# Kernel optimization log

Measured on AMD Instinct MI355X. Metric: run time of the kernel, lower is better.

Reference implementation:

```python
import jax, jax.numpy as jnp
import numpy as np

V = 5023          # FLAME vertex count
NJ = 5            # joints: global, neck, jaw, eyeL, eyeR
N_SHAPE = 100
N_EXP = 50
PARENTS = np.array([-1, 0, 1, 1, 1], dtype=np.int64)  # static kintree
N_BATCH = 2048


def setup_inputs() -> dict:
    key = jax.random.key(0)
    ks = jax.random.split(key, 12)
    N = N_BATCH
    shape = jax.random.normal(ks[0], (N, N_SHAPE), jnp.float32)
    exp = jax.random.normal(ks[1], (N, N_EXP), jnp.float32)
    neck_pose = 0.1 * jax.random.normal(ks[2], (N, 3), jnp.float32)
    jaw_pose = 0.1 * jax.random.normal(ks[3], (N, 3), jnp.float32)
    eye_pose = 0.1 * jax.random.normal(ks[4], (N, 6), jnp.float32)
    v_template = jax.random.normal(ks[5], (V, 3), jnp.float32)
    shapedirs = 0.01 * jax.random.normal(ks[6], (V, 3, N_SHAPE + N_EXP), jnp.float32)
    posedirs = 0.01 * jax.random.normal(ks[7], (36, V * 3), jnp.float32)
    J_regressor = jax.random.uniform(ks[8], (NJ, V), jnp.float32)
    J_regressor = J_regressor / J_regressor.sum(axis=1, keepdims=True)
    lbs_weights = jax.random.uniform(ks[9], (V, NJ), jnp.float32)
    lbs_weights = lbs_weights / lbs_weights.sum(axis=1, keepdims=True)
    parents = jnp.asarray(PARENTS)
    return dict(shape=shape, exp=exp, neck_pose=neck_pose, jaw_pose=jaw_pose,
                eye_pose=eye_pose, v_template=v_template, shapedirs=shapedirs,
                posedirs=posedirs, J_regressor=J_regressor, lbs_weights=lbs_weights,
                parents=parents)


def rodrigues(rot_vecs):
    """Axis-angle [...,3] -> rotation matrices [...,3,3] (matches SMPL/FLAME impl)."""
    angle = jnp.linalg.norm(rot_vecs + 1e-8, axis=-1, keepdims=True)
    rd = rot_vecs / angle
    cos = jnp.cos(angle)[..., None]
    sin = jnp.sin(angle)[..., None]
    rx, ry, rz = rd[..., 0], rd[..., 1], rd[..., 2]
    z = jnp.zeros_like(rx)
    K = jnp.stack([z, -rz, ry, rz, z, -rx, -ry, rx, z], axis=-1).reshape(rd.shape + (3,))
    I = jnp.eye(3, dtype=rot_vecs.dtype)
    return I + sin * K + (1.0 - cos) * (K @ K)


def flame_forward(shape, exp, neck_pose, jaw_pose, eye_pose, v_template,
                  shapedirs, posedirs, J_regressor, lbs_weights):
    N = shape.shape[0]
    dt = shape.dtype
    betas = jnp.concatenate([shape, exp], axis=1)                      # [N,150]
    # full pose: zeroed global rot + neck + jaw + eyes -> [N,NJ,3]
    full_pose = jnp.concatenate([jnp.zeros_like(jaw_pose), neck_pose,
                                 jaw_pose, eye_pose], axis=1).reshape(N, NJ, 3)
    # shape blendshapes
    v_shaped = v_template[None] + jnp.einsum('bl,vkl->bvk', betas, shapedirs)  # [N,V,3]
    J = jnp.einsum('jv,bvk->bjk', J_regressor, v_shaped)               # [N,NJ,3]
    # pose blendshapes
    R = rodrigues(full_pose)                                           # [N,NJ,3,3]
    pose_feature = (R[:, 1:] - jnp.eye(3, dtype=dt)).reshape(N, (NJ - 1) * 9)
    v_posed = v_shaped + (pose_feature @ posedirs).reshape(N, V, 3)
    # kinematic chain (static 5-joint tree)
    rel_J = J.at[:, 1:].add(-J[:, PARENTS[1:]])
    Rt = jnp.concatenate([R, rel_J[..., None]], axis=-1)               # [N,NJ,3,4]
    bottom = jnp.broadcast_to(jnp.array([0., 0., 0., 1.], dtype=dt), (N, NJ, 1, 4))
    T = jnp.concatenate([Rt, bottom], axis=2)                          # [N,NJ,4,4]
    chain = [T[:, 0]]
    for i in range(1, NJ):
        chain.append(chain[int(PARENTS[i])] @ T[:, i])
    G = jnp.stack(chain, axis=1)                                       # [N,NJ,4,4]
    # remove rest-pose joint locations from the transforms
    J_h = jnp.concatenate([J, jnp.zeros((N, NJ, 1), dt)], axis=-1)     # [N,NJ,4]
    t_corr = jnp.einsum('bjrc,bjc->bjr', G, J_h)
    A = G.at[..., 3].add(-t_corr)                                      # [N,NJ,4,4]
    # linear blend skinning
    Tw = jnp.einsum('vj,bjrc->bvrc', lbs_weights, A)                   # [N,V,4,4]
    v_h = jnp.concatenate([v_posed, jnp.ones((N, V, 1), dt)], axis=-1)
    verts = jnp.einsum('bvrc,bvc->bvr', Tw, v_h)[..., :3]              # [N,V,3]
    return verts


def reference(shape, exp, neck_pose, jaw_pose, eye_pose, v_template,
              shapedirs, posedirs, J_regressor, lbs_weights, parents):
    # parents is a static buffer (PARENTS) -- accepted for signature parity.
    return flame_forward(shape, exp, neck_pose, jaw_pose, eye_pose, v_template,
                         shapedirs, posedirs, J_regressor, lbs_weights)
```

## Files before the change

kernel.cpp:

```cpp
#include <hip/hip_runtime.h>
#include <hip/hip_bf16.h>
#include <math.h>

#define NV   5023
#define N3   15069
#define NB   2048
#define NTIL 79
#define NPAD (NTIL*192)

#define WS_JD_B   0
#define WS_ATR_B  9216
#define WS_AB_B   795648
#define WS_BB_B   1582080

#define GP_J 126
#define GP_S 1067
#define GP_P 237

typedef __attribute__((ext_vector_type(8))) short short8;
typedef __attribute__((ext_vector_type(4))) float floatx4;

static __device__ __forceinline__ unsigned short f2bf(float x) {
    union { __hip_bfloat16 h; unsigned short s; } u;
    u.h = __float2bfloat16(x);
    return u.s;
}
static __device__ __forceinline__ unsigned int pk2(float a, float b) {
    return (unsigned int)f2bf(a) | ((unsigned int)f2bf(b) << 16);
}

#define BAR_LGKM() do { \
    asm volatile("s_waitcnt lgkmcnt(0)" ::: "memory"); \
    __builtin_amdgcn_s_barrier(); \
    asm volatile("" ::: "memory"); \
} while (0)

__global__ void k_prep(const float* __restrict__ Jreg,
                       const float* __restrict__ sdirs,
                       const float* __restrict__ vt,
                       const float* __restrict__ pdirs,
                       char* __restrict__ ws) {
    __shared__ float JregL[200];
    __shared__ float PL[36][65];
    const int t = threadIdx.x;

    if (blockIdx.x < GP_J) {
        int slice = blockIdx.x;
        int start = slice * 40;
        int end   = min(start + 40, NV);
        if (t < 200) {
            int j = t / 40, vl = t % 40;
            int v = start + vl;
            JregL[t] = (v < NV) ? Jreg[j * NV + v] : 0.f;
        }
        __syncthreads();
        int s0 = t, s1 = t + 256;
        float a0[5] = {0,0,0,0,0}, a1[5] = {0,0,0,0,0};
        #pragma unroll 2
        for (int v = start; v < end; ++v) {
            int vl = v - start;
            float x0 = (s0 < 450) ? sdirs[(size_t)v * 450 + s0]
                     : (s0 < 453 ? vt[v * 3 + (s0 - 450)] : 0.f);
            float x1 = (s1 < 450) ? sdirs[(size_t)v * 450 + s1]
                     : (s1 < 453 ? vt[v * 3 + (s1 - 450)] : 0.f);
            #pragma unroll
            for (int j = 0; j < 5; ++j) {
                float w = JregL[j * 40 + vl];
                a0[j] += w * x0; a1[j] += w * x1;
            }
        }
        float* Jd = (float*)(ws + WS_JD_B);
        #pragma unroll
        for (int j = 0; j < 5; ++j) {
            if (s0 < 453) atomicAdd(&Jd[j * 453 + s0], a0[j]);
            if (s1 < 453) atomicAdd(&Jd[j * 453 + s1], a1[j]);
        }
    } else if (blockIdx.x < GP_J + GP_S) {
        int idx = (blockIdx.x - GP_J) * 256 + t;
        if (idx < NPAD * 18) {
            int n = idx / 18, g = idx % 18;
            __hip_bfloat16* dst = (__hip_bfloat16*)(ws + WS_BB_B) + (size_t)n * 192 + g * 8;
            if (n < N3) {
                const float* src = sdirs + (size_t)n * 150 + g * 8;
                float2 p0 = *(const float2*)(src);
                float2 p1 = *(const float2*)(src + 2);
                float2 p2 = *(const float2*)(src + 4);
                float2 p3 = *(const float2*)(src + 6);
                unsigned int w[4] = { pk2(p0.x, p0.y), pk2(p1.x, p1.y),
                                      pk2(p2.x, p2.y), pk2(p3.x, p3.y) };
                *(int4*)dst = *(int4*)w;
            } else {
                int4 z = {0, 0, 0, 0};
                *(int4*)dst = z;
            }
        }
    } else {
        int pb = blockIdx.x - (GP_J + GP_S);
        int n0 = pb * 64;
        #pragma unroll
        for (int j = 0; j < 9; ++j) {
            int flat = j * 256 + t;
            int k = flat >> 6, i = flat & 63;
            int n = n0 + i;
            PL[k][i] = (n < N3) ? pdirs[(size_t)k * N3 + n] : 0.f;
        }
        __syncthreads();
        #pragma unroll
        for (int j = 0; j < 2; ++j) {
            int idx2 = j * 256 + t;
            if (idx2 < 384) {
                int r = idx2 / 6, g = idx2 % 6;
                int n = n0 + r;
                int k0 = 144 + g * 8;
                __hip_bfloat16 val[8];
                #pragma unroll
                for (int e = 0; e < 8; ++e) {
                    int k = k0 + e;
                    float v = 0.f;
                    if (k < 150)      v = (n < N3) ? sdirs[(size_t)n * 150 + k] : 0.f;
                    else if (k < 186) v = PL[k - 150][r];
                    val[e] = __float2bfloat16(v);
                }
                *(int4*)((__hip_bfloat16*)(ws + WS_BB_B) + (size_t)n * 192 + k0) = *(int4*)val;
            }
        }
    }
}

static __device__ __forceinline__ void rodr3(float rx, float ry, float rz, float* R) {
    float ax = rx + 1e-8f, ay = ry + 1e-8f, az = rz + 1e-8f;
    float angle = sqrtf(ax*ax + ay*ay + az*az);
    float inv = 1.f / angle;
    float ux = rx * inv, uy = ry * inv, uz = rz * inv;
    float c = cosf(angle), s = sinf(angle);
    float K[9] = {0.f, -uz, uy,  uz, 0.f, -ux,  -uy, ux, 0.f};
    float KK[9];
    #pragma unroll
    for (int r = 0; r < 3; ++r)
        #pragma unroll
        for (int cc = 0; cc < 3; ++cc) {
            float a = 0.f;
            #pragma unroll
            for (int m = 0; m < 3; ++m) a += K[r*3+m] * K[m*3+cc];
            KK[r*3+cc] = a;
        }
    #pragma unroll
    for (int e = 0; e < 9; ++e) R[e] = s * K[e] + (1.f - c) * KK[e];
    R[0] += 1.f; R[4] += 1.f; R[8] += 1.f;
}

#define KBS 0
#define KBE 6464
#define KBJ 9728
#define KBR 11993
#define KBP 16345
#define KBT 18713

__global__ __launch_bounds__(256) void k_batch(
        const float* __restrict__ shp,
        const float* __restrict__ expn,
        const float* __restrict__ neck,
        const float* __restrict__ jaw,
        const float* __restrict__ eye,
        char* __restrict__ ws) {
    __shared__ float L[KBT];
    const int t  = threadIdx.x;
    const int b0 = blockIdx.x * 64;

    {
        const float* Jd = (const float*)(ws + WS_JD_B);
        for (int i = t; i < 6400; i += 256) { int r = i / 100, c = i - r * 100; L[KBS + r*101 + c] = shp[(size_t)b0*100 + i]; }
        for (int i = t; i < 3200; i += 256) { int r = i / 50,  c = i - r * 50;  L[KBE + r*51  + c] = expn[(size_t)b0*50 + i]; }
        for (int i = t; i < 2265; i += 256) L[KBJ + i] = Jd[i];
    }
    __syncthreads();

    const int br = t & 63, seg = t >> 6;
    {
        float Jp[15];
        #pragma unroll
        for (int u = 0; u < 15; ++u) Jp[u] = 0.f;
        int l0 = seg * 38, l1 = (seg == 3) ? 150 : (l0 + 38);
        for (int l = l0; l < l1; ++l) {
            float be = (l < 100) ? L[KBS + br*101 + l] : L[KBE + br*51 + (l - 100)];
            #pragma unroll
            for (int jj = 0; jj < 5; ++jj)
                #pragma unroll
                for (int kk = 0; kk < 3; ++kk)
                    Jp[jj*3 + kk] += L[KBJ + jj*453 + kk*150 + l] * be;
        }
        #pragma unroll
        for (int u = 0; u < 15; ++u) L[KBR + (seg*64 + br)*17 + u] = Jp[u];
    }
    __syncthreads();

    if (t < 64) {
        int b = b0 + t;
        float J[15];
        #pragma unroll
        for (int jk = 0; jk < 15; ++jk) {
            float s = L[KBJ + (jk/3)*453 + 450 + (jk%3)];
            #pragma unroll
            for (int sg = 0; sg < 4; ++sg) s += L[KBR + (sg*64 + t)*17 + jk];
            J[jk] = s;
        }

        float R[4][9];
        rodr3(neck[b*3], neck[b*3+1], neck[b*3+2], R[0]);
        rodr3(jaw[b*3],  jaw[b*3+1],  jaw[b*3+2],  R[1]);
        rodr3(eye[b*6],  eye[b*6+1],  eye[b*6+2],  R[2]);
        rodr3(eye[b*6+3], eye[b*6+4], eye[b*6+5],  R[3]);

        #pragma unroll
        for (int kk2 = 0; kk2 < 4; ++kk2)
            #pragma unroll
            for (int e = 0; e < 9; ++e)
                L[KBP + t*37 + kk2*9 + e] = R[kk2][e] - ((e == 0 || e == 4 || e == 8) ? 1.f : 0.f);

        float* Atr = (float*)(ws + WS_ATR_B) + (size_t)b * 60;
        Atr[0]=1.f; Atr[1]=0.f; Atr[2]=0.f;  Atr[3]=0.f;
        Atr[4]=0.f; Atr[5]=1.f; Atr[6]=0.f;  Atr[7]=0.f;
        Atr[8]=0.f; Atr[9]=0.f; Atr[10]=1.f; Atr[11]=0.f;
        #pragma unroll
        for (int r = 0; r < 3; ++r) {
            float d = R[0][r*3+0]*J[3] + R[0][r*3+1]*J[4] + R[0][r*3+2]*J[5];
            Atr[12 + r*4 + 0] = R[0][r*3+0];
            Atr[12 + r*4 + 1] = R[0][r*3+1];
            Atr[12 + r*4 + 2] = R[0][r*3+2];
            Atr[12 + r*4 + 3] = J[3+r] - d;
        }
        #pragma unroll
        for (int kk = 1; kk < 4; ++kk) {
            int jj = kk + 1;
            float rel[3];
            #pragma unroll
            for (int r = 0; r < 3; ++r) rel[r] = J[jj*3+r] - J[3+r];
            float Gr[9], tv[3];
            #pragma unroll
            for (int r = 0; r < 3; ++r) {
                #pragma unroll
                for (int cc = 0; cc < 3; ++cc) {
                    float a = 0.f;
                    #pragma unroll
                    for (int m = 0; m < 3; ++m) a += R[0][r*3+m] * R[kk][m*3+cc];
                    Gr[r*3+cc] = a;
                }
                tv[r] = R[0][r*3+0]*rel[0] + R[0][r*3+1]*rel[1] + R[0][r*3+2]*rel[2] + J[3+r];
            }
            #pragma unroll
            for (int r = 0; r < 3; ++r) {
                float d = Gr[r*3+0]*J[jj*3+0] + Gr[r*3+1]*J[jj*3+1] + Gr[r*3+2]*J[jj*3+2];
                Atr[jj*12 + r*4 + 0] = Gr[r*3+0];
                Atr[jj*12 + r*4 + 1] = Gr[r*3+1];
                Atr[jj*12 + r*4 + 2] = Gr[r*3+2];
                Atr[jj*12 + r*4 + 3] = tv[r] - d;
            }
        }
    }
    __syncthreads();

    unsigned int* A32g = (unsigned int*)(ws + WS_AB_B);
    for (int i = t; i < 6144; i += 256) {
        int r = i / 96, w = i - r * 96;
        unsigned int val;
        if (w < 50)      val = pk2(L[KBS + r*101 + 2*w],     L[KBS + r*101 + 2*w + 1]);
        else if (w < 75) { int c = 2*(w-50); val = pk2(L[KBE + r*51 + c], L[KBE + r*51 + c + 1]); }
        else if (w < 93) { int c = 2*(w-75); val = pk2(L[KBP + r*37 + c], L[KBP + r*37 + c + 1]); }
        else             val = 0u;
        A32g[(size_t)(b0 + r)*96 + w] = val;
    }
}

#define A_OFF  0
#define B_OFF  4352
#define S_VT   17
#define S_AT   61
#define VT_T_OFF 0
#define ATR_OFF  13056
#define VTQ_OFF  16960
#define LBS_OFF  17728
#define SMEM_BYTES 30464

__global__ __launch_bounds__(256, 5) void k_mega(
        const char* __restrict__ ws,
        const float* __restrict__ vt,
        const float* __restrict__ lbsw,
        float* __restrict__ out) {
    __shared__ __align__(16) unsigned char smem[SMEM_BYTES];
    const unsigned char* AbG = (const unsigned char*)ws + WS_AB_B;
    const unsigned char* BbG = (const unsigned char*)ws + WS_BB_B;
    const float* AtrG = (const float*)(ws + WS_ATR_B);

    const int ntile = blockIdx.y;
    const int b0    = blockIdx.x * 32;
    const int t     = threadIdx.x;
    const int lane  = t & 63;
    const int wn    = t >> 6;
    const int l15 = lane & 15, quad = lane >> 4;

    floatx4 acc[2][3];
    #pragma unroll
    for (int f = 0; f < 2; ++f)
        #pragma unroll
        for (int g = 0; g < 3; ++g) {
            floatx4 z = {0.f, 0.f, 0.f, 0.f};
            acc[f][g] = z;
        }

    for (int chunk = 0; chunk < 3; ++chunk) {
        __syncthreads();
        {
            int row = t >> 3, piece = t & 7;
            *(float4*)(smem + A_OFF + row * 136 + piece * 16) =
                *(const float4*)(AbG + (size_t)(b0 + row) * 384 + chunk * 128 + piece * 16);
        }
        #pragma unroll
        for (int i = 0; i < 6; ++i) {
            int flat = i * 256 + t;
            int row = flat >> 3, piece = flat & 7;
            *(float4*)(smem + B_OFF + row * 136 + piece * 16) =
                *(const float4*)(BbG + (size_t)(ntile * 192 + row) * 384 + chunk * 128 + piece * 16);
        }
        __syncthreads();
        #pragma unroll
        for (int ks = 0; ks < 2; ++ks) {
            short8 af[2];
            #pragma unroll
            for (int f = 0; f < 2; ++f)
                af[f] = *(const short8*)(smem + A_OFF + (f * 16 + l15) * 136 + ks * 64 + quad * 16);
            #pragma unroll
            for (int g = 0; g < 3; ++g) {
                short8 bf = *(const short8*)(smem + B_OFF + (wn * 48 + g * 16 + l15) * 136 + ks * 64 + quad * 16);
                #pragma unroll
                for (int f = 0; f < 2; ++f)
                    acc[f][g] = __builtin_amdgcn_mfma_f32_16x16x32_bf16(af[f], bf, acc[f][g], 0, 0, 0);
            }
        }
    }
    __syncthreads();

    float* vtT  = (float*)(smem + VT_T_OFF);
    float* atrS = (float*)(smem + ATR_OFF);
    float* vtQ  = (float*)(smem + VTQ_OFF);
    float* lbsS = (float*)(smem + LBS_OFF);

    if (t < 192) { int n = ntile * 192 + t; vtQ[t] = (n < N3) ? vt[n] : 0.f; }
    for (int i = t; i < 320; i += 256) {
        int v = ntile * 64 + i / 5;
        lbsS[i] = (v < NV) ? lbsw[(size_t)v * 5 + (i % 5)] : 0.f;
    }
    float arA[4], arB[4];
    #pragma unroll
    for (int u = 0; u < 4; ++u) {
        int i = u * 256 + t;
        arA[u] = (i < 960) ? AtrG[(size_t)b0 * 60 + i] : 0.f;
    }

    #define EPI_PHASE(HH, ARCUR, PRELOAD_NEXT)                                          \
    {                                                                                   \
        BAR_LGKM();                                                                     \
                                   \
        _Pragma("unroll")                                                               \
        for (int g = 0; g < 3; ++g) {                                                   \
            int col = wn * 48 + g * 16 + l15;                                           \
            int rl  = quad * 4;                                                         \
            _Pragma("unroll")                                                           \
            for (int r = 0; r < 4; ++r)                                                 \
                vtT[col * S_VT + rl + r] = acc[HH][g][r];                               \
        }                                                                               \
                                                         \
        _Pragma("unroll")                                                               \
        for (int u = 0; u < 4; ++u) {                                                   \
            int i = u * 256 + t;                                                        \
            if (i < 960) {                                                              \
                int rw = i / 60, cw = i - rw * 60;                                      \
                atrS[rw * S_AT + cw] = ARCUR[u];                                        \
            }                                                                           \
        }                                                                               \
        PRELOAD_NEXT                                                                    \
        BAR_LGKM();                                                                     \
                          \
        {                                                                               \
            int rl = t & 15;                                                            \
            int vgrp = t >> 4;                                                          \
            float ar[60];                                                               \
            _Pragma("unroll")                                                           \
            for (int i = 0; i < 60; ++i) ar[i] = atrS[rl * S_AT + i];                   \
            _Pragma("unroll")                                                           \
            for (int vv = 0; vv < 4; ++vv) {                                            \
                int vloc = vgrp * 4 + vv;                                               \
                int c0 = vloc * 3;                                                      \
                float w0 = lbsS[vloc*5+0], w1 = lbsS[vloc*5+1], w2 = lbsS[vloc*5+2],    \
                      w3 = lbsS[vloc*5+3], w4 = lbsS[vloc*5+4];                         \
                float px = vtT[(c0+0) * S_VT + rl] + vtQ[c0+0];                         \
                float py = vtT[(c0+1) * S_VT + rl] + vtQ[c0+1];                         \
                float pz = vtT[(c0+2) * S_VT + rl] + vtQ[c0+2];                         \
                float y[3];                                                             \
                _Pragma("unroll")                                                       \
                for (int r = 0; r < 3; ++r) {                                           \
                    float t0 = w0*ar[ 0+r*4+0] + w1*ar[12+r*4+0] + w2*ar[24+r*4+0]      \
                             + w3*ar[36+r*4+0] + w4*ar[48+r*4+0];                       \
                    float t1 = w0*ar[ 0+r*4+1] + w1*ar[12+r*4+1] + w2*ar[24+r*4+1]      \
                             + w3*ar[36+r*4+1] + w4*ar[48+r*4+1];                       \
                    float t2 = w0*ar[ 0+r*4+2] + w1*ar[12+r*4+2] + w2*ar[24+r*4+2]      \
                             + w3*ar[36+r*4+2] + w4*ar[48+r*4+2];                       \
                    float t3 = w0*ar[ 0+r*4+3] + w1*ar[12+r*4+3] + w2*ar[24+r*4+3]      \
                             + w3*ar[36+r*4+3] + w4*ar[48+r*4+3];                       \
                    y[r] = t0*px + t1*py + t2*pz + t3;                                  \
                }                                                                       \
                vtT[(c0+0) * S_VT + rl] = y[0];                                         \
                vtT[(c0+1) * S_VT + rl] = y[1];                                         \
                vtT[(c0+2) * S_VT + rl] = y[2];                                         \
            }                                                                           \
        }                                                                               \
        BAR_LGKM();                                                                     \
                  \
        {                                                                               \
            int wv = t >> 6;                                                            \
            const bool full = (ntile * 192 + 192 <= N3);                                \
            for (int rr = wv; rr < 16; rr += 4) {                                       \
                size_t ob = (size_t)(b0 + HH * 16 + rr) * N3 + (size_t)ntile * 192;     \
                if (full) {                                                             \
                    _Pragma("unroll")                                                   \
                    for (int e = 0; e < 3; ++e) {                                       \
                        int col = e * 64 + lane;                                        \
                        out[ob + col] = vtT[col * S_VT + rr];                           \
                    }                                                                   \
                } else {                                                                \
                    _Pragma("unroll")                                                   \
                    for (int e = 0; e < 3; ++e) {                                       \
                        int col = e * 64 + lane;                                        \
                        if (ntile * 192 + col < N3)                                     \
                            out[ob + col] = vtT[col * S_VT + rr];                       \
                    }                                                                   \
                }                                                                       \
            }                                                                           \
        }                                                                               \
    }

    EPI_PHASE(0, arA,
        { _Pragma("unroll")
          for (int u = 0; u < 4; ++u) {
              int i = u * 256 + t;
              arB[u] = (i < 960) ? AtrG[(size_t)(b0 + 16) * 60 + i] : 0.f;
          } } )
    EPI_PHASE(1, arB, { } )
    #undef EPI_PHASE
}

extern "C" void kernel_launch(void* const* d_in, const int* in_sizes, int n_in,
                              void* d_out, int out_size, void* d_ws, size_t ws_size,
                              hipStream_t stream) {
    const float* shp  = (const float*)d_in[0];
    const float* expn = (const float*)d_in[1];
    const float* neck = (const float*)d_in[2];
    const float* jaw  = (const float*)d_in[3];
    const float* eye  = (const float*)d_in[4];
    const float* vt   = (const float*)d_in[5];
    const float* sdir = (const float*)d_in[6];
    const float* pdir = (const float*)d_in[7];
    const float* jreg = (const float*)d_in[8];
    const float* lbsw = (const float*)d_in[9];
    char* ws  = (char*)d_ws;
    float* out = (float*)d_out;

    hipMemsetAsync(ws + WS_JD_B, 0, 2272 * 4, stream);
    k_prep <<<GP_J + GP_S + GP_P, 256, 0, stream>>>(jreg, sdir, vt, pdir, ws);
    k_batch<<<32, 256, 0, stream>>>(shp, expn, neck, jaw, eye, ws);
    k_mega <<<dim3(64, NTIL), 256, 0, stream>>>(ws, vt, lbsw, out);
}
```

Baseline: 262.9 us.

## Skin epilogue with wave-uniform transform loads instead of LDS-staged transforms

Reworks the skinning epilogue so each lane owns one vertex and each wave handles batch rows. The per-row 60-float joint transform is read straight from global memory through a readfirstlane-uniform pointer as float4 (scalar-cacheable), replacing the LDS staging of transforms and the 60-register per-thread copy. The LBS weights and template offsets are hoisted into registers once. This removes LDS traffic, a staging pass and register pressure, but relies on cached global loads and drops the prefetch overlap of the next half's transforms.

```diff
diff --git a/kernel.cpp b/kernel.cpp
--- a/kernel.cpp
+++ b/kernel.cpp
@@ -274,11 +274,9 @@
 #define A_OFF  0
 #define B_OFF  4352
 #define S_VT   17
-#define S_AT   61
 #define VT_T_OFF 0
-#define ATR_OFF  13056
-#define VTQ_OFF  16960
-#define LBS_OFF  17728
+#define VTQ_OFF  13056
+#define LBS_OFF  13824
 #define SMEM_BYTES 30464
 
 __global__ __launch_bounds__(256, 5) void k_mega(
@@ -340,7 +338,6 @@
     __syncthreads();
 
     float* vtT  = (float*)(smem + VT_T_OFF);
-    float* atrS = (float*)(smem + ATR_OFF);
     float* vtQ  = (float*)(smem + VTQ_OFF);
     float* lbsS = (float*)(smem + LBS_OFF);
 
@@ -349,103 +346,74 @@
         int v = ntile * 64 + i / 5;
         lbsS[i] = (v < NV) ? lbsw[(size_t)v * 5 + (i % 5)] : 0.f;
     }
-    float arA[4], arB[4];
+    BAR_LGKM();
+
+    float wj0 = lbsS[lane*5+0], wj1 = lbsS[lane*5+1], wj2 = lbsS[lane*5+2],
+          wj3 = lbsS[lane*5+3], wj4 = lbsS[lane*5+4];
+    float vq0 = vtQ[lane*3+0], vq1 = vtQ[lane*3+1], vq2 = vtQ[lane*3+2];
+
     #pragma unroll
-    for (int u = 0; u < 4; ++u) {
-        int i = u * 256 + t;
-        arA[u] = (i < 960) ? AtrG[(size_t)b0 * 60 + i] : 0.f;
-    }
-
-    #define EPI_PHASE(HH, ARCUR, PRELOAD_NEXT)                                          \
-    {                                                                                   \
-        BAR_LGKM();                                                                     \
-                                   \
-        _Pragma("unroll")                                                               \
-        for (int g = 0; g < 3; ++g) {                                                   \
-            int col = wn * 48 + g * 16 + l15;                                           \
-            int rl  = quad * 4;                                                         \
-            _Pragma("unroll")                                                           \
-            for (int r = 0; r < 4; ++r)                                                 \
-                vtT[col * S_VT + rl + r] = acc[HH][g][r];                               \
-        }                                                                               \
-                                                         \
-        _Pragma("unroll")                                                               \
-        for (int u = 0; u < 4; ++u) {                                                   \
-            int i = u * 256 + t;                                                        \
-            if (i < 960) {                                                              \
-                int rw = i / 60, cw = i - rw * 60;                                      \
-                atrS[rw * S_AT + cw] = ARCUR[u];                                        \
-            }                                                                           \
-        }                                                                               \
-        PRELOAD_NEXT                                                                    \
-        BAR_LGKM();                                                                     \
-                          \
-        {                                                                               \
-            int rl = t & 15;                                                            \
-            int vgrp = t >> 4;                                                          \
-            float ar[60];                                                               \
-            _Pragma("unroll")                                                           \
-            for (int i = 0; i < 60; ++i) ar[i] = atrS[rl * S_AT + i];                   \
-            _Pragma("unroll")                                                           \
-            for (int vv = 0; vv < 4; ++vv) {                                            \
-                int vloc = vgrp * 4 + vv;                                               \
-                int c0 = vloc * 3;                                                      \
-                float w0 = lbsS[vloc*5+0], w1 = lbsS[vloc*5+1], w2 = lbsS[vloc*5+2],    \
-                      w3 = lbsS[vloc*5+3], w4 = lbsS[vloc*5+4];                         \
-                float px = vtT[(c0+0) * S_VT + rl] + vtQ[c0+0];                         \
-                float py = vtT[(c0+1) * S_VT + rl] + vtQ[c0+1];                         \
-                float pz = vtT[(c0+2) * S_VT + rl] + vtQ[c0+2];                         \
-                float y[3];                                                             \
-                _Pragma("unroll")                                                       \
-                for (int r = 0; r < 3; ++r) {                                           \
-                    float t0 = w0*ar[ 0+r*4+0] + w1*ar[12+r*4+0] + w2*ar[24+r*4+0]      \
-                             + w3*ar[36+r*4+0] + w4*ar[48+r*4+0];                       \
-                    float t1 = w0*ar[ 0+r*4+1] + w1*ar[12+r*4+1] + w2*ar[24+r*4+1]      \
-                             + w3*ar[36+r*4+1] + w4*ar[48+r*4+1];                       \
-                    float t2 = w0*ar[ 0+r*4+2] + w1*ar[12+r*4+2] + w2*ar[24+r*4+2]      \
-                             + w3*ar[36+r*4+2] + w4*ar[48+r*4+2];                       \
-                    float t3 = w0*ar[ 0+r*4+3] + w1*ar[12+r*4+3] + w2*ar[24+r*4+3]      \
-                             + w3*ar[36+r*4+3] + w4*ar[48+r*4+3];                       \
-                    y[r] = t0*px + t1*py + t2*pz + t3;                                  \
-                }                                                                       \
-                vtT[(c0+0) * S_VT + rl] = y[0];                                         \
-                vtT[(c0+1) * S_VT + rl] = y[1];                                         \
-                vtT[(c0+2) * S_VT + rl] = y[2];                                         \
-            }                                                                           \
-        }                                                                               \
-        BAR_LGKM();                                                                     \
-                  \
-        {                                                                               \
-            int wv = t >> 6;                                                            \
-            const bool full = (ntile * 192 + 192 <= N3);                                \
-            for (int rr = wv; rr < 16; rr += 4) {                                       \
-                size_t ob = (size_t)(b0 + HH * 16 + rr) * N3 + (size_t)ntile * 192;     \
-                if (full) {                                                             \
-                    _Pragma("unroll")                                                   \
-                    for (int e = 0; e < 3; ++e) {                                       \
-                        int col = e * 64 + lane;                                        \
-                        out[ob + col] = vtT[col * S_VT + rr];                           \
-                    }                                                                   \
-                } else {                                                                \
-                    _Pragma("unroll")                                                   \
-                    for (int e = 0; e < 3; ++e) {                                       \
-                        int col = e * 64 + lane;                                        \
-                        if (ntile * 192 + col < N3)                                     \
-                            out[ob + col] = vtT[col * S_VT + rr];                       \
-                    }                                                                   \
-                }                                                                       \
-            }                                                                           \
-        }                                                                               \
-    }
-
-    EPI_PHASE(0, arA,
-        { _Pragma("unroll")
-          for (int u = 0; u < 4; ++u) {
-              int i = u * 256 + t;
-              arB[u] = (i < 960) ? AtrG[(size_t)(b0 + 16) * 60 + i] : 0.f;
-          } } )
-    EPI_PHASE(1, arB, { } )
-    #undef EPI_PHASE
+    for (int HH = 0; HH < 2; ++HH) {
+        if (HH) BAR_LGKM();
+        #pragma unroll
+        for (int g = 0; g < 3; ++g) {
+            int col = wn * 48 + g * 16 + l15;
+            int rl  = quad * 4;
+            #pragma unroll
+            for (int r = 0; r < 4; ++r)
+                vtT[col * S_VT + rl + r] = acc[HH][g][r];
+        }
+        BAR_LGKM();
+
+        #pragma unroll
+        for (int i = 0; i < 4; ++i) {
+            int row = wn * 4 + i;
+            int rowg = __builtin_amdgcn_readfirstlane(b0 + HH * 16 + row);
+            const float* ar = AtrG + (size_t)rowg * 60;
+            float px = vtT[(lane*3+0) * S_VT + row] + vq0;
+            float py = vtT[(lane*3+1) * S_VT + row] + vq1;
+            float pz = vtT[(lane*3+2) * S_VT + row] + vq2;
+            float y[3];
+            #pragma unroll
+            for (int r = 0; r < 3; ++r) {
+                float4 a0 = *(const float4*)(ar +  0 + r*4);
+                float4 a1 = *(const float4*)(ar + 12 + r*4);
+                float4 a2 = *(const float4*)(ar + 24 + r*4);
+                float4 a3 = *(const float4*)(ar + 36 + r*4);
+                float4 a4 = *(const float4*)(ar + 48 + r*4);
+                float t0 = wj0*a0.x + wj1*a1.x + wj2*a2.x + wj3*a3.x + wj4*a4.x;
+                float t1 = wj0*a0.y + wj1*a1.y + wj2*a2.y + wj3*a3.y + wj4*a4.y;
+                float t2 = wj0*a0.z + wj1*a1.z + wj2*a2.z + wj3*a3.z + wj4*a4.z;
+                float t3 = wj0*a0.w + wj1*a1.w + wj2*a2.w + wj3*a3.w + wj4*a4.w;
+                y[r] = t0*px + t1*py + t2*pz + t3;
+            }
+            vtT[(lane*3+0) * S_VT + row] = y[0];
+            vtT[(lane*3+1) * S_VT + row] = y[1];
+            vtT[(lane*3+2) * S_VT + row] = y[2];
+        }
+        BAR_LGKM();
+
+        {
+            const bool full = (ntile * 192 + 192 <= N3);
+            for (int rr = wn; rr < 16; rr += 4) {
+                size_t ob = (size_t)(b0 + HH * 16 + rr) * N3 + (size_t)ntile * 192;
+                if (full) {
+                    #pragma unroll
+                    for (int e = 0; e < 3; ++e) {
+                        int col = e * 64 + lane;
+                        out[ob + col] = vtT[col * S_VT + rr];
+                    }
+                } else {
+                    #pragma unroll
+                    for (int e = 0; e < 3; ++e) {
+                        int col = e * 64 + lane;
+                        if (ntile * 192 + col < N3)
+                            out[ob + col] = vtT[col * S_VT + rr];
+                    }
+                }
+            }
+        }
+    }
 }
 
 extern "C" void kernel_launch(void* const* d_in, const int* in_sizes, int n_in,
```

After: 292.4 us. +11.3%, slower.
